# Optimization experiments

Hardware: AMD Instinct MI355X
Metric: run time of the kernel (lower is better)

## Reference

```python
import jax, jax.numpy as jnp
import numpy as np

N_NODES = 100000
N_EDGES = 1600000
HIDDEN = 128
LAYERS = 2


def setup_inputs() -> dict:
    key = jax.random.key(0)
    k1, k2, k3, k4 = jax.random.split(key, 4)
    x = jax.random.normal(k1, (N_NODES, HIDDEN), dtype=jnp.float32)
    edge_index = jax.random.randint(k2, (2, N_EDGES), 0, N_NODES, dtype=jnp.int32)
    # Glorot-ish init for per-layer GCN weights, small bias
    Ws = jax.random.normal(k3, (LAYERS, HIDDEN, HIDDEN), dtype=jnp.float32) / np.sqrt(HIDDEN).astype(np.float32)
    bs = jax.random.normal(k4, (LAYERS, HIDDEN), dtype=jnp.float32) * 0.01
    return {"x": x, "edge_index": edge_index, "Ws": Ws, "bs": bs}


def reference(x, edge_index, Ws, bs):
    # PyG GCNConv with normalize=True, add_self_loops=False:
    #   x' = D^{-1/2} A D^{-1/2} (x W) + b,  deg = in-degree at target (col) nodes
    src = edge_index[0]  # message sources (row)
    dst = edge_index[1]  # message targets (col), aggregation index
    ones = jnp.ones(src.shape[0], dtype=x.dtype)
    deg = jax.ops.segment_sum(ones, dst, num_segments=N_NODES)
    dinv = jnp.where(deg > 0, jax.lax.rsqrt(jnp.maximum(deg, 1.0)), jnp.zeros_like(deg))
    norm = dinv[src] * dinv[dst]  # [E] symmetric edge normalization
    for l in range(Ws.shape[0]):
        h = x @ Ws[l]                                  # [N, D] dense transform
        msg = h[src] * norm[:, None]                   # [E, D] gather + scale
        x = jax.ops.segment_sum(msg, dst, num_segments=N_NODES) + bs[l]
    return x
```

## Files before the change

kernel.cpp:

```cpp
#include <hip/hip_runtime.h>

#define HID 128
#define WFRAG (HID*HID)
#define NXCD 8

typedef __attribute__((ext_vector_type(8))) short bf16x8;
typedef __attribute__((ext_vector_type(4))) float f32x4;

static __device__ __forceinline__ unsigned short f2bf(float f){
  unsigned u = __float_as_uint(f);
  unsigned r = (u + 0x7FFF + ((u >> 16) & 1)) >> 16;
  return (unsigned short)r;
}
static __device__ __forceinline__ float bf2f_lo(unsigned u){ return __uint_as_float(u << 16); }
static __device__ __forceinline__ float bf2f_hi(unsigned u){ return __uint_as_float(u & 0xFFFF0000u); }

static __device__ __forceinline__ unsigned cvtpk(float lo, float hi){
  unsigned r;
  asm volatile("v_cvt_pk_bf16_f32 %0, %1, %2" : "=v"(r) : "v"(lo), "v"(hi));
  return r;
}

__global__ __launch_bounds__(256) void k_wprep(const float* __restrict__ Ws,
                                               unsigned short* __restrict__ Whi,
                                               unsigned short* __restrict__ Wlo){
  int layer = blockIdx.x;
  const float* W = Ws + (size_t)layer*HID*HID;
  for (int idx = threadIdx.x; idx < 2048; idx += 256){
    int lane = idx & 63, kstep = (idx>>6)&3, nblk = idx>>8;
    int col = 16*nblk + (lane&15);
    int k0  = 32*kstep + 8*(lane>>4);
    size_t obase = ((size_t)(layer*8 + nblk)*4 + kstep)*512 + (size_t)lane*8;
    for (int j = 0; j < 8; j++){
      float v = W[(size_t)(k0+j)*HID + col];
      unsigned short h = f2bf(v);
      float hf = __uint_as_float((unsigned)h << 16);
      Whi[obase+j] = h;
      Wlo[obase+j] = f2bf(v - hf);
    }
  }
}

__global__ __launch_bounds__(256) void k_pos8(const int* __restrict__ dst, int* __restrict__ fill8,
                                              int* __restrict__ pos, int E, int N){
  int xcc = __builtin_amdgcn_s_getreg((31<<11) | 20) & (NXCD-1);
  int e = blockIdx.x*256 + threadIdx.x;
  if (e < E){
    int d = dst[e];
    int p = atomicAdd(&fill8[(size_t)xcc*N + d], 1);
    pos[e] = (xcc << 28) | p;
  }
}

__global__ __launch_bounds__(256) void k_alloc8(const int* __restrict__ fill8, int* __restrict__ deg,
                                                int* __restrict__ rowstart, int* __restrict__ xbase,
                                                float* __restrict__ dinv, int* __restrict__ cursor, int N){
  __shared__ int sm[256];
  __shared__ int sbase;
  int t = threadIdx.x;
  int n = blockIdx.x*256 + t;
  int c[NXCD];
  int d = 0;
  if (n < N){
#pragma unroll
    for (int x = 0; x < NXCD; x++){ c[x] = fill8[(size_t)x*N + n]; d += c[x]; }
  }
  sm[t] = d;
  __syncthreads();
  for (int off = 1; off < 256; off <<= 1){
    int v = (t >= off) ? sm[t-off] : 0;
    __syncthreads();
    sm[t] += v;
    __syncthreads();
  }
  if (t == 255) sbase = atomicAdd(cursor, sm[255]);
  __syncthreads();
  if (n < N){
    int rs = sbase + sm[t] - d;
    rowstart[n] = rs;
    deg[n] = d;
    dinv[n] = d > 0 ? rsqrtf((float)d) : 0.0f;
    int xb = rs;
#pragma unroll
    for (int x = 0; x < NXCD; x++){ xbase[(size_t)x*N + n] = xb; xb += c[x]; }
  }
}

static __device__ __forceinline__ void gemm_body_f32(int bid, const float* __restrict__ X,
                                                     const unsigned short* __restrict__ Whi,
                                                     const unsigned short* __restrict__ Wlo,
                                                     unsigned short* __restrict__ H2u, int N){
  int t = threadIdx.x, w = t>>6, l = t&63;
  int row0 = bid*32;
  int lrow = l & 15, lk = (l>>4)*8;
  f32x4 acc[2][2] = {};
#pragma unroll 1
  for (int kstep = 0; kstep < 4; kstep++){
    bf16x8 ahi[2], alo[2];
#pragma unroll
    for (int m = 0; m < 2; m++){
      int row = row0 + 16*m + lrow;
      if (row >= N) row = N-1;
      const float* ap = X + (size_t)row*HID + kstep*32 + lk;
      float4 a0 = *(const float4*)ap;
      float4 a1 = *(const float4*)(ap+4);
      int4 hh, ll;
      hh.x = cvtpk(a0.x, a0.y); hh.y = cvtpk(a0.z, a0.w);
      hh.z = cvtpk(a1.x, a1.y); hh.w = cvtpk(a1.z, a1.w);
      ll.x = cvtpk(a0.x - bf2f_lo(hh.x), a0.y - bf2f_hi(hh.x));
      ll.y = cvtpk(a0.z - bf2f_lo(hh.y), a0.w - bf2f_hi(hh.y));
      ll.z = cvtpk(a1.x - bf2f_lo(hh.z), a1.y - bf2f_hi(hh.z));
      ll.w = cvtpk(a1.z - bf2f_lo(hh.w), a1.w - bf2f_hi(hh.w));
      ahi[m] = *(bf16x8*)&hh;
      alo[m] = *(bf16x8*)&ll;
    }
#pragma unroll
    for (int n = 0; n < 2; n++){
      size_t base = ((size_t)((2*w+n)*4 + kstep))*512 + (size_t)l*8;
      bf16x8 bhi = *(const bf16x8*)(Whi + base);
      bf16x8 blo = *(const bf16x8*)(Wlo + base);
#pragma unroll
      for (int m = 0; m < 2; m++){
        acc[m][n] = __builtin_amdgcn_mfma_f32_16x16x32_bf16(ahi[m], bhi, acc[m][n], 0, 0, 0);
        acc[m][n] = __builtin_amdgcn_mfma_f32_16x16x32_bf16(alo[m], bhi, acc[m][n], 0, 0, 0);
        acc[m][n] = __builtin_amdgcn_mfma_f32_16x16x32_bf16(ahi[m], blo, acc[m][n], 0, 0, 0);
      }
    }
  }
#pragma unroll
  for (int m = 0; m < 2; m++)
#pragma unroll
    for (int r = 0; r < 4; r++){
      int row = row0 + 16*m + 4*(l>>4) + r;
      if (row < N){
#pragma unroll
        for (int n = 0; n < 2; n++){
          int col = 16*(2*w+n) + lrow;
          H2u[(size_t)row*HID + col] = f2bf(acc[m][n][r]);
        }
      }
    }
}

__global__ __launch_bounds__(256) void k_gemm0_scatter(const float* __restrict__ X,
                                                       const unsigned short* __restrict__ Whi,
                                                       const unsigned short* __restrict__ Wlo,
                                                       unsigned short* __restrict__ H2u, int N, int Gg,
                                                       const int* __restrict__ src, const int* __restrict__ dst,
                                                       const int* __restrict__ pos, const int* __restrict__ xbase,
                                                       const float* __restrict__ dinv,
                                                       int2* __restrict__ slots, int E){
  int bid = blockIdx.x;
  if (bid < Gg){ gemm_body_f32(bid, X, Whi, Wlo, H2u, N); return; }
  int i0 = ((bid - Gg)*256 + threadIdx.x)*2;
  if (i0 + 1 < E){
    int2 s = *(const int2*)(src + i0);
    int2 d = *(const int2*)(dst + i0);
    int2 p = *(const int2*)(pos + i0);
    int slot0 = xbase[(size_t)(p.x >> 28)*N + d.x] + (p.x & 0x0FFFFFFF);
    int slot1 = xbase[(size_t)(p.y >> 28)*N + d.y] + (p.y & 0x0FFFFFFF);
    slots[slot0] = make_int2(s.x, __float_as_int(dinv[s.x]));
    slots[slot1] = make_int2(s.y, __float_as_int(dinv[s.y]));
  } else if (i0 < E){
    int s = src[i0], d = dst[i0], p = pos[i0];
    slots[xbase[(size_t)(p >> 28)*N + d] + (p & 0x0FFFFFFF)] = make_int2(s, __float_as_int(dinv[s]));
  }
}

__global__ __launch_bounds__(256) void k_gemm_bf16(const unsigned short* __restrict__ Xb,
                                                   const unsigned short* __restrict__ Whi,
                                                   const unsigned short* __restrict__ Wlo,
                                                   unsigned short* __restrict__ H2u, int N){
  int t = threadIdx.x, w = t>>6, l = t&63;
  int row0 = blockIdx.x*32;
  int lrow = l & 15, lk = (l>>4)*8;
  f32x4 acc[2][2] = {};
#pragma unroll 1
  for (int kstep = 0; kstep < 4; kstep++){
    bf16x8 a[2];
#pragma unroll
    for (int m = 0; m < 2; m++){
      int row = row0 + 16*m + lrow;
      if (row >= N) row = N-1;
      a[m] = *(const bf16x8*)(Xb + (size_t)row*HID + kstep*32 + lk);
    }
#pragma unroll
    for (int n = 0; n < 2; n++){
      size_t base = ((size_t)((2*w+n)*4 + kstep))*512 + (size_t)l*8;
      bf16x8 bhi = *(const bf16x8*)(Whi + base);
      bf16x8 blo = *(const bf16x8*)(Wlo + base);
#pragma unroll
      for (int m = 0; m < 2; m++){
        acc[m][n] = __builtin_amdgcn_mfma_f32_16x16x32_bf16(a[m], bhi, acc[m][n], 0, 0, 0);
        acc[m][n] = __builtin_amdgcn_mfma_f32_16x16x32_bf16(a[m], blo, acc[m][n], 0, 0, 0);
      }
    }
  }
#pragma unroll
  for (int m = 0; m < 2; m++)
#pragma unroll
    for (int r = 0; r < 4; r++){
      int row = row0 + 16*m + 4*(l>>4) + r;
      if (row < N){
#pragma unroll
        for (int n = 0; n < 2; n++){
          int col = 16*(2*w+n) + lrow;
          H2u[(size_t)row*HID + col] = f2bf(acc[m][n][r]);
        }
      }
    }
}

template<int OUTBF>
__global__ __launch_bounds__(256) void k_agg(const uint4* __restrict__ H4, const int2* __restrict__ slots,
                                             const int* __restrict__ rowstart, const int* __restrict__ deg,
                                             const float* __restrict__ dinv,
                                             const float* __restrict__ bias, void* __restrict__ outp, int N){
  int wid = threadIdx.x >> 6, lane = threadIdx.x & 63;
  int n = blockIdx.x*4 + wid;
  if (n >= N) return;
  int st = rowstart[n], cnt = deg[n];
  int g = lane >> 4, c = lane & 15;
  float a[8] = {0.f,0.f,0.f,0.f,0.f,0.f,0.f,0.f};
  for (int j = 0; j < cnt; j += 16){
    int cl = cnt - 1;
    int2 sl[4];
#pragma unroll
    for (int q = 0; q < 4; q++){
      int jj = j + 4*q + g;
      sl[q] = slots[st + (jj < cnt ? jj : cl)];
    }
    uint4 v[4];
#pragma unroll
    for (int q = 0; q < 4; q++) v[q] = H4[(size_t)sl[q].x*16 + c];
#pragma unroll
    for (int q = 0; q < 4; q++){
      float wq = (j + 4*q + g < cnt) ? __int_as_float(sl[q].y) : 0.f;
      a[0] += wq*bf2f_lo(v[q].x);
      a[1] += wq*bf2f_hi(v[q].x);
      a[2] += wq*bf2f_lo(v[q].y);
      a[3] += wq*bf2f_hi(v[q].y);
      a[4] += wq*bf2f_lo(v[q].z);
      a[5] += wq*bf2f_hi(v[q].z);
      a[6] += wq*bf2f_lo(v[q].w);
      a[7] += wq*bf2f_hi(v[q].w);
    }
  }
#pragma unroll
  for (int q = 0; q < 8; q++){
    a[q] += __shfl_xor(a[q], 16);
    a[q] += __shfl_xor(a[q], 32);
  }
  if (g == 0){
    float dv = dinv[n];
    const float4* b4 = (const float4*)bias;
    float4 b0 = b4[c*2], b1 = b4[c*2+1];
    float o[8];
    o[0]=dv*a[0]+b0.x; o[1]=dv*a[1]+b0.y; o[2]=dv*a[2]+b0.z; o[3]=dv*a[3]+b0.w;
    o[4]=dv*a[4]+b1.x; o[5]=dv*a[5]+b1.y; o[6]=dv*a[6]+b1.z; o[7]=dv*a[7]+b1.w;
    if (OUTBF){
      uint4 p;
      p.x = (unsigned)f2bf(o[0]) | ((unsigned)f2bf(o[1]) << 16);
      p.y = (unsigned)f2bf(o[2]) | ((unsigned)f2bf(o[3]) << 16);
      p.z = (unsigned)f2bf(o[4]) | ((unsigned)f2bf(o[5]) << 16);
      p.w = (unsigned)f2bf(o[6]) | ((unsigned)f2bf(o[7]) << 16);
      ((uint4*)outp)[(size_t)n*16 + c] = p;
    } else {
      float4* orow = (float4*)((float*)outp + (size_t)n*HID);
      orow[c*2]   = make_float4(o[0],o[1],o[2],o[3]);
      orow[c*2+1] = make_float4(o[4],o[5],o[6],o[7]);
    }
  }
}

extern "C" void kernel_launch(void* const* d_in, const int* in_sizes, int n_in,
                              void* d_out, int out_size, void* d_ws, size_t ws_size,
                              hipStream_t stream){
  const float* x  = (const float*)d_in[0];
  const int*   ei = (const int*)d_in[1];
  const float* Ws = (const float*)d_in[2];
  const float* bs = (const float*)d_in[3];
  const int N = in_sizes[0] / HID;
  const int E = in_sizes[1] / 2;
  const int L = in_sizes[2] / (HID*HID);
  const int* src = ei;
  const int* dst = ei + E;
  const int NB = (N + 255)/256;

  char* w = (char*)d_ws;
  int*   fill8    = (int*)w;   w += (size_t)NXCD*N*4;
  int*   cursor   = (int*)w;   w += 16;
  size_t zbytes = (size_t)(w - (char*)d_ws);
  int*   deg      = (int*)w;   w += (size_t)N*4;
  float* dinv     = (float*)w; w += (size_t)N*4;
  int*   rowstart = (int*)w;   w += (size_t)N*4;
  int*   xbase    = (int*)w;   w += (size_t)NXCD*N*4;
  int*   pos      = (int*)w;   w += (size_t)E*4;
  int2*  slots    = (int2*)w;  w += (size_t)E*8 + 64;
  unsigned short* h2u = (unsigned short*)w; w += (size_t)N*HID*2;
  unsigned short* xb1 = (unsigned short*)w; w += (size_t)N*HID*2;
  unsigned short* whi = (unsigned short*)w; w += (size_t)L*WFRAG*2;
  unsigned short* wlo = (unsigned short*)w; w += (size_t)L*WFRAG*2;

  hipMemsetAsync(d_ws, 0, zbytes, stream);

  int Gp = (E + 255)/256;
  int Gs = (E/2 + 255)/256 + 1;
  int Gg = (N + 31)/32;
  int Ga = (N + 3)/4;

  k_wprep <<<L, 256, 0, stream>>>(Ws, whi, wlo);
  k_pos8  <<<Gp, 256, 0, stream>>>(dst, fill8, pos, E, N);
  k_alloc8<<<NB, 256, 0, stream>>>(fill8, deg, rowstart, xbase, dinv, cursor, N);
  k_gemm0_scatter<<<Gg + Gs, 256, 0, stream>>>(x, whi, wlo, h2u, N, Gg,
                                               src, dst, pos, xbase, dinv, slots, E);
  k_agg<1><<<Ga, 256, 0, stream>>>((const uint4*)h2u, slots, rowstart, deg,
                                   dinv, bs, (void*)xb1, N);
  k_gemm_bf16<<<Gg, 256, 0, stream>>>(xb1, whi + WFRAG, wlo + WFRAG, h2u, N);
  k_agg<0><<<Ga, 256, 0, stream>>>((const uint4*)h2u, slots, rowstart, deg,
                                   dinv, bs + HID, d_out, N);
}
```

Measured before the change: 326.6 us.

## Partition CSR slot scatter by destination range per XCD with chunk work queues

Merges the weight-prep kernel into the position-counting kernel, removing one launch. Replaces the flat per-edge slot scatter with persistent blocks that pull edge chunks from per-XCD atomic queues. Each XCD handles only the destinations in its own node range, so slot writes stay local to that XCD's L2. The cost is that every XCD now reads the full dst array and filters it, which multiplies dst reads by eight and adds queue atomics and block barriers.

Result: slower. 345.6 us (+5.8%).

```diff
diff --git a/kernel.cpp b/kernel.cpp
--- a/kernel.cpp
+++ b/kernel.cpp
@@ -3,6 +3,7 @@
 #define HID 128
 #define WFRAG (HID*HID)
 #define NXCD 8
+#define CHUNK 4096
 
 typedef __attribute__((ext_vector_type(8))) short bf16x8;
 typedef __attribute__((ext_vector_type(4))) float f32x4;
@@ -21,10 +22,13 @@
   return r;
 }
 
-__global__ __launch_bounds__(256) void k_wprep(const float* __restrict__ Ws,
-                                               unsigned short* __restrict__ Whi,
-                                               unsigned short* __restrict__ Wlo){
-  int layer = blockIdx.x;
+static __device__ __forceinline__ int xccid(){
+  return __builtin_amdgcn_s_getreg((31<<11) | 20) & (NXCD-1);
+}
+
+static __device__ __forceinline__ void wprep_body(int layer, const float* __restrict__ Ws,
+                                                  unsigned short* __restrict__ Whi,
+                                                  unsigned short* __restrict__ Wlo){
   const float* W = Ws + (size_t)layer*HID*HID;
   for (int idx = threadIdx.x; idx < 2048; idx += 256){
     int lane = idx & 63, kstep = (idx>>6)&3, nblk = idx>>8;
@@ -41,14 +45,19 @@
   }
 }
 
-__global__ __launch_bounds__(256) void k_pos8(const int* __restrict__ dst, int* __restrict__ fill8,
-                                              int* __restrict__ pos, int E, int N){
-  int xcc = __builtin_amdgcn_s_getreg((31<<11) | 20) & (NXCD-1);
-  int e = blockIdx.x*256 + threadIdx.x;
+__global__ __launch_bounds__(256) void k_wprep_pos8(const float* __restrict__ Ws,
+                                                    unsigned short* __restrict__ Whi,
+                                                    unsigned short* __restrict__ Wlo, int L,
+                                                    const int* __restrict__ dst, int* __restrict__ fill8,
+                                                    int* __restrict__ pos, int E, int N){
+  int bid = blockIdx.x;
+  if (bid < L){ wprep_body(bid, Ws, Whi, Wlo); return; }
+  int e = (bid - L)*256 + threadIdx.x;
   if (e < E){
+    int x = xccid();
     int d = dst[e];
-    int p = atomicAdd(&fill8[(size_t)xcc*N + d], 1);
-    pos[e] = (xcc << 28) | p;
+    int p = atomicAdd(&fill8[(size_t)x*N + d], 1);
+    pos[e] = (x << 28) | p;
   }
 }
 
@@ -142,28 +151,39 @@
     }
 }
 
-__global__ __launch_bounds__(256) void k_gemm0_scatter(const float* __restrict__ X,
-                                                       const unsigned short* __restrict__ Whi,
-                                                       const unsigned short* __restrict__ Wlo,
-                                                       unsigned short* __restrict__ H2u, int N, int Gg,
-                                                       const int* __restrict__ src, const int* __restrict__ dst,
-                                                       const int* __restrict__ pos, const int* __restrict__ xbase,
-                                                       const float* __restrict__ dinv,
-                                                       int2* __restrict__ slots, int E){
+__global__ __launch_bounds__(256) void k_gemm0_xscatter(const float* __restrict__ X,
+                                                        const unsigned short* __restrict__ Whi,
+                                                        const unsigned short* __restrict__ Wlo,
+                                                        unsigned short* __restrict__ H2u, int N, int Gg,
+                                                        const int* __restrict__ src, const int* __restrict__ dst,
+                                                        const int* __restrict__ pos, const int* __restrict__ xbase,
+                                                        const float* __restrict__ dinv,
+                                                        int2* __restrict__ slots, int E,
+                                                        int* __restrict__ qcur, int nchunks, int Rsz){
   int bid = blockIdx.x;
   if (bid < Gg){ gemm_body_f32(bid, X, Whi, Wlo, H2u, N); return; }
-  int i0 = ((bid - Gg)*256 + threadIdx.x)*2;
-  if (i0 + 1 < E){
-    int2 s = *(const int2*)(src + i0);
-    int2 d = *(const int2*)(dst + i0);
-    int2 p = *(const int2*)(pos + i0);
-    int slot0 = xbase[(size_t)(p.x >> 28)*N + d.x] + (p.x & 0x0FFFFFFF);
-    int slot1 = xbase[(size_t)(p.y >> 28)*N + d.y] + (p.y & 0x0FFFFFFF);
-    slots[slot0] = make_int2(s.x, __float_as_int(dinv[s.x]));
-    slots[slot1] = make_int2(s.y, __float_as_int(dinv[s.y]));
-  } else if (i0 < E){
-    int s = src[i0], d = dst[i0], p = pos[i0];
-    slots[xbase[(size_t)(p >> 28)*N + d] + (p & 0x0FFFFFFF)] = make_int2(s, __float_as_int(dinv[s]));
+  __shared__ int smc;
+  int myx = xccid();
+  for (int xo = 0; xo < NXCD; xo++){
+    int x = (myx + xo) & (NXCD-1);
+    int lo = x*Rsz, hi = lo + Rsz < N ? lo + Rsz : N;
+    while (true){
+      if (threadIdx.x == 0) smc = atomicAdd(&qcur[x*16], 1);
+      __syncthreads();
+      int chunk = smc;
+      __syncthreads();
+      if (chunk >= nchunks) break;
+      int e0 = chunk*CHUNK;
+      int e1 = e0 + CHUNK < E ? e0 + CHUNK : E;
+      for (int i = e0 + threadIdx.x; i < e1; i += 256){
+        int d = dst[i];
+        if (d >= lo && d < hi){
+          int p = pos[i], s = src[i];
+          slots[xbase[(size_t)(p >> 28)*N + d] + (p & 0x0FFFFFFF)] =
+              make_int2(s, __float_as_int(dinv[s]));
+        }
+      }
+    }
   }
 }
 
@@ -289,7 +309,8 @@
 
   char* w = (char*)d_ws;
   int*   fill8    = (int*)w;   w += (size_t)NXCD*N*4;
-  int*   cursor   = (int*)w;   w += 16;
+  int*   cursor   = (int*)w;   w += 64;
+  int*   qcur     = (int*)w;   w += NXCD*16*4;
   size_t zbytes = (size_t)(w - (char*)d_ws);
   int*   deg      = (int*)w;   w += (size_t)N*4;
   float* dinv     = (float*)w; w += (size_t)N*4;
@@ -305,15 +326,16 @@
   hipMemsetAsync(d_ws, 0, zbytes, stream);
 
   int Gp = (E + 255)/256;
-  int Gs = (E/2 + 255)/256 + 1;
   int Gg = (N + 31)/32;
   int Ga = (N + 3)/4;
-
-  k_wprep <<<L, 256, 0, stream>>>(Ws, whi, wlo);
-  k_pos8  <<<Gp, 256, 0, stream>>>(dst, fill8, pos, E, N);
-  k_alloc8<<<NB, 256, 0, stream>>>(fill8, deg, rowstart, xbase, dinv, cursor, N);
-  k_gemm0_scatter<<<Gg + Gs, 256, 0, stream>>>(x, whi, wlo, h2u, N, Gg,
-                                               src, dst, pos, xbase, dinv, slots, E);
+  int nchunks = (E + CHUNK - 1)/CHUNK;
+  int Rsz = (N + NXCD - 1)/NXCD;
+
+  k_wprep_pos8<<<L + Gp, 256, 0, stream>>>(Ws, whi, wlo, L, dst, fill8, pos, E, N);
+  k_alloc8    <<<NB, 256, 0, stream>>>(fill8, deg, rowstart, xbase, dinv, cursor, N);
+  k_gemm0_xscatter<<<Gg + 2048, 256, 0, stream>>>(x, whi, wlo, h2u, N, Gg,
+                                                  src, dst, pos, xbase, dinv, slots, E,
+                                                  qcur, nchunks, Rsz);
   k_agg<1><<<Ga, 256, 0, stream>>>((const uint4*)h2u, slots, rowstart, deg,
                                    dinv, bs, (void*)xb1, N);
   k_gemm_bf16<<<Gg, 256, 0, stream>>>(xb1, whi + WFRAG, wlo + WFRAG, h2u, N);
```
